# Performance work log

Hardware: AMD Instinct MI355X
Metric: run time of the kernel (lower is better)

Reference implementation:

```python
import jax, jax.numpy as jnp
import numpy as np
from jax import lax

B, C, D, NH, H, W = 32, 768, 512, 4, 24, 24
HD = C // NH          # 192
FHW = H * W           # 576 (must equal 24*24 per o_proj_img2)


def _p(key, shape, scale=0.02):
    return scale * jax.random.normal(key, shape, dtype=jnp.float32)


def setup_inputs() -> dict:
    ks = jax.random.split(jax.random.key(0), 10)
    return dict(
        img_feats=jax.random.normal(ks[0], (B, C, H, W), jnp.float32),
        txt_feats=jax.random.normal(ks[1], (B, D), jnp.float32),
        fn_w=jnp.ones((C,), jnp.float32), fn_b=jnp.zeros((C,), jnp.float32),
        gn_w=jnp.ones((D,), jnp.float32), gn_b=jnp.zeros((D,), jnp.float32),
        qkv_img_w=_p(ks[2], (3 * C, C)),
        qkv_txt_w=_p(ks[3], (3 * C, D)),
        o_img_w=_p(ks[4], (C, C)), o_img_b=jnp.zeros((C,), jnp.float32),
        o_img2_w=_p(ks[5], (FHW, HD)), o_img2_b=jnp.zeros((FHW,), jnp.float32),
        ffn_norm_w=jnp.ones((C,), jnp.float32), ffn_norm_b=jnp.zeros((C,), jnp.float32),
        fc1_w=_p(ks[6], (C, C)),
        dw_w=_p(ks[7], (C, 1, 3, 3)),
        fc2_w=_p(ks[8], (C, C)),
    )


def layernorm2d(x, w, b, eps=1e-6):
    # normalize over channel dim (dim 1) of NCHW
    u = x.mean(1, keepdims=True)
    s = ((x - u) ** 2).mean(1, keepdims=True)
    x = (x - u) * lax.rsqrt(s + eps)
    return w[:, None, None] * x + b[:, None, None]


def l2norm_last(x, eps=1e-12):
    # F.normalize(x, dim=-1): divide by L2 norm clamped at eps
    n = jnp.sqrt(jnp.sum(x * x, axis=-1, keepdims=True))
    return x / jnp.maximum(n, eps)


def _forward(img_feats, txt_feats, fn_w, fn_b, gn_w, gn_b, qkv_img_w, qkv_txt_w,
             o_img_w, o_img_b, o_img2_w, o_img2_b, ffn_norm_w, ffn_norm_b,
             fc1_w, dw_w, fc2_w):
    x = layernorm2d(img_feats, fn_w, fn_b)
    # guide LayerNorm (torch default eps=1e-5, biased var)
    mu = txt_feats.mean(-1, keepdims=True)
    var = jnp.mean((txt_feats - mu) ** 2, axis=-1, keepdims=True)
    t = (txt_feats - mu) * lax.rsqrt(var + 1e-5) * gn_w + gn_b

    # qkv img: 1x1 conv; channel layout (ng nh hd) -> [B,3,NH,HD,F]
    qkv_img = jnp.einsum('bchw,oc->bohw', x, qkv_img_w).reshape(B, 3, NH, HD, FHW)
    q_img, k_img, v_img = qkv_img[:, 0], qkv_img[:, 1], qkv_img[:, 2]

    # qkv txt: layout 'b (nh (ng hd))' per the two rearranges -> [B,NH,3,HD]
    qkv_txt = (t @ qkv_txt_w.T).reshape(B, NH, 3, HD)
    q_txt, k_txt = qkv_txt[:, :, 0], qkv_txt[:, :, 1]

    # normalize over size-1 trailing dim == x / max(|x|, eps)  (sign-like)
    nq_txt = q_txt / jnp.maximum(jnp.abs(q_txt), 1e-12)          # [B,NH,HD]
    nk_img = l2norm_last(k_img)                                  # [B,NH,HD,F]
    # einsum('bnhd,bnhf->bnhf') with d of size 1 == broadcast multiply over h
    attn1 = jax.nn.softmax(nq_txt[..., None] * nk_img, axis=-1)  # [B,NH,HD,F]
    txt_on_img = jnp.einsum('bnhf,bngf->bnhg', attn1, v_img)     # [B,NH,HD,HD]

    nk_txt = k_txt / jnp.maximum(jnp.abs(k_txt), 1e-12)
    nq_img = l2norm_last(q_img)
    attn2 = jax.nn.softmax(nk_txt[..., None] * nq_img, axis=-1)
    txt_to_img2 = jnp.einsum('bnhf,bngf->bnhg', attn2, v_img)

    img = (txt_on_img + txt_to_img2).reshape(B, NH * HD, HD)     # [B,768,192]
    y = (img @ o_img2_w.T + o_img2_b).reshape(B, C, H, W)        # [B,768,24,24]
    out = jnp.einsum('bchw,oc->bohw', y, o_img_w) + o_img_b[None, :, None, None] + img_feats

    # ConvMlp FFN (mlp_times=1, bias=False convs, exact GELU)
    z = layernorm2d(out, ffn_norm_w, ffn_norm_b)
    z = jnp.einsum('bchw,oc->bohw', z, fc1_w)
    z = lax.conv_general_dilated(z, dw_w, (1, 1), 'SAME',
                                 feature_group_count=C,
                                 dimension_numbers=('NCHW', 'OIHW', 'NCHW'))
    z = jax.nn.gelu(z, approximate=False)
    z = jnp.einsum('bchw,oc->bohw', z, fc2_w)
    return out + z


def reference(img_feats, txt_feats, fn_w, fn_b, gn_w, gn_b, qkv_img_w, qkv_txt_w,
              o_img_w, o_img_b, o_img2_w, o_img2_b, ffn_norm_w, ffn_norm_b,
              fc1_w, dw_w, fc2_w):
    return _forward(img_feats, txt_feats, fn_w, fn_b, gn_w, gn_b, qkv_img_w,
                    qkv_txt_w, o_img_w, o_img_b, o_img2_w, o_img2_b,
                    ffn_norm_w, ffn_norm_b, fc1_w, dw_w, fc2_w)
```

## Files before the change

### kernel.cpp

```cpp
#include <hip/hip_runtime.h>

typedef unsigned short u16;
typedef __attribute__((ext_vector_type(8))) short short8_t;
typedef __attribute__((ext_vector_type(4))) float f32x4;

static constexpr int cB   = 32;
static constexpr int cC   = 768;
static constexpr int cD   = 512;
static constexpr int cNH  = 4;
static constexpr int cHD  = 192;
static constexpr int cFHW = 576;
static constexpr int cC3  = 2304;

__device__ inline float us2f(u16 s) {
    union { unsigned int u; float f; } v; v.u = ((unsigned int)s) << 16; return v.f;
}
__device__ inline u16 f2bf(float f) {
    union { float f; unsigned int u; } v; v.f = f;
    unsigned int r = v.u + 0x7FFFu + ((v.u >> 16) & 1u);
    return (u16)(r >> 16);
}
__device__ inline float ldflex(const void* p, size_t i, int isf32) {
    return isf32 ? ((const float*)p)[i] : us2f(((const u16*)p)[i]);
}

__device__ inline void gload16(const void* g, void* l) {
    __builtin_amdgcn_global_load_lds(
        (const __attribute__((address_space(1))) void*)g,
        (__attribute__((address_space(3))) void*)l, 16, 0, 0);
}

__global__ void detect_kernel(const u16* __restrict__ raw, int* __restrict__ flags) {
    flags[0] = (raw[0] == 0x3F80u) ? 0 : 1;
}

struct FlatDesc { const void* src[12]; float* dst[12]; int off[13]; };
__global__ __launch_bounds__(256) void flatten_kernel(FlatDesc d, const int* __restrict__ flags) {
    const int isf = flags[0];
    const int gid = blockIdx.x * 256 + threadIdx.x;
    if (gid >= d.off[12]) return;
    int s = 0;
    #pragma unroll
    for (int i = 1; i < 12; i++) s += (gid >= d.off[i]) ? 1 : 0;
    const int j = gid - d.off[s];
    d.dst[s][j] = ldflex(d.src[s], j, isf);
}

__global__ __launch_bounds__(256) void cast_bf16_kernel(
    const void* __restrict__ src, u16* __restrict__ dst, int n, const int* __restrict__ flags)
{
    const int isf = flags[0];
    for (int i = blockIdx.x * 256 + threadIdx.x; i < n; i += gridDim.x * 256)
        dst[i] = isf ? f2bf(((const float*)src)[i]) : ((const u16*)src)[i];
}

__global__ __launch_bounds__(256) void transpose_kernel(
    const void* __restrict__ src, float* __restrict__ dst,
    int Mdim, int Kdim, const int* __restrict__ flags)
{
    __shared__ float t[32][33];
    const int isf = flags[0];
    const int k0 = blockIdx.x * 32, m0 = blockIdx.y * 32;
    const int x = threadIdx.x & 31, y = threadIdx.x >> 5;
    #pragma unroll
    for (int i = 0; i < 4; i++) {
        const int m = y + i * 8;
        t[m][x] = ldflex(src, (size_t)(m0 + m) * Kdim + k0 + x, isf);
    }
    __syncthreads();
    #pragma unroll
    for (int i = 0; i < 4; i++) {
        const int r = y + i * 8;
        dst[(size_t)(k0 + r) * Mdim + m0 + x] = t[x][r];
    }
}

__global__ __launch_bounds__(256) void txt_ln_kernel(
    const float* __restrict__ txt, const float* __restrict__ gw, const float* __restrict__ gb,
    float* __restrict__ tln)
{
    __shared__ float red[8];
    const int b = blockIdx.x, tid = threadIdx.x;
    const float v0 = txt[(size_t)b * cD + tid];
    const float v1 = txt[(size_t)b * cD + 256 + tid];
    float s = v0 + v1, ss = v0 * v0 + v1 * v1;
    #pragma unroll
    for (int o = 1; o < 64; o <<= 1) { s += __shfl_xor(s, o, 64); ss += __shfl_xor(ss, o, 64); }
    const int wid = tid >> 6, lane = tid & 63;
    if (lane == 0) { red[wid] = s; red[4 + wid] = ss; }
    __syncthreads();
    s  = red[0] + red[1] + red[2] + red[3];
    ss = red[4] + red[5] + red[6] + red[7];
    const float mean = s * (1.f / cD);
    const float var  = fmaxf(ss * (1.f / cD) - mean * mean, 0.f);
    const float r = rsqrtf(var + 1e-5f);
    tln[(size_t)b * cD + tid]       = (v0 - mean) * r * gw[tid]       + gb[tid];
    tln[(size_t)b * cD + 256 + tid] = (v1 - mean) * r * gw[tid + 256] + gb[tid + 256];
}

__global__ __launch_bounds__(256) void txt_gemm_kernel(
    const float* __restrict__ Wt, const float* __restrict__ tln, float* __restrict__ out)
{
    const int o  = blockIdx.x * 256 + threadIdx.x;
    const int b0 = blockIdx.y * 8;
    __shared__ float t[8][cD];
    for (int i = threadIdx.x; i < 8 * cD; i += 256)
        t[i >> 9][i & (cD - 1)] = tln[(size_t)(b0 + (i >> 9)) * cD + (i & (cD - 1))];
    __syncthreads();
    float acc[8] = {};
    #pragma unroll 2
    for (int k = 0; k < cD; k += 4) {
        const float w0 = Wt[(size_t)(k + 0) * cC3 + o];
        const float w1 = Wt[(size_t)(k + 1) * cC3 + o];
        const float w2 = Wt[(size_t)(k + 2) * cC3 + o];
        const float w3 = Wt[(size_t)(k + 3) * cC3 + o];
        #pragma unroll
        for (int b = 0; b < 8; b++) {
            const float4 tv = *(const float4*)&t[b][k];
            acc[b] += w0 * tv.x + w1 * tv.y + w2 * tv.z + w3 * tv.w;
        }
    }
    #pragma unroll
    for (int b = 0; b < 8; b++) out[(size_t)(b0 + b) * cC3 + o] = acc[b];
}

template <int RAW>
__global__ __launch_bounds__(1024) void ln_stats_kernel(
    const void* __restrict__ x, size_t xoff, float* __restrict__ mr,
    const int* __restrict__ flags)
{
    const int isf = RAW ? flags[0] : 1;
    const int b = blockIdx.y;
    const int l = threadIdx.x & 63;
    const int f = (blockIdx.x << 6) + l;
    const int cg = threadIdx.x >> 6;
    const size_t base = (size_t)b * cC * cFHW + f;
    const size_t rbase = RAW ? (xoff + base) : base;
    float s = 0.f, ss = 0.f;
    for (int c = cg; c < cC; c += 16) {
        float v = RAW ? ldflex(x, rbase + (size_t)c * cFHW, isf)
                      : ((const float*)x)[base + (size_t)c * cFHW];
        s += v; ss += v * v;
    }
    __shared__ float S[16][64], SS[16][64];
    S[cg][l] = s; SS[cg][l] = ss;
    __syncthreads();
    if (threadIdx.x < 64) {
        float su = 0.f, sq = 0.f;
        #pragma unroll
        for (int i = 0; i < 16; i++) { su += S[i][l]; sq += SS[i][l]; }
        const float mean = su * (1.f / cC);
        const float var  = fmaxf(sq * (1.f / cC) - mean * mean, 0.f);
        float* o = mr + ((size_t)b * cFHW + f) * 2;
        o[0] = mean; o[1] = rsqrtf(var + 1e-6f);
    }
}

template <int XSRC>
__global__ __launch_bounds__(256) void prep_xt_kernel(
    const void* __restrict__ X, size_t xoff, u16* __restrict__ Xt,
    const float* __restrict__ mr, const float* __restrict__ lnw, const float* __restrict__ lnb,
    const int* __restrict__ flags)
{
    __shared__ float t[64][33];
    const int isf = (XSRC == 2) ? flags[0] : 1;
    const int f0 = blockIdx.x * 32, c0 = blockIdx.y * 64, b = blockIdx.z;
    const int tid = threadIdx.x;
    const int fx = tid & 31, cy = tid >> 5;
    const size_t base = (size_t)b * cC * cFHW;
    #pragma unroll
    for (int i = 0; i < 8; i++) {
        const int c = c0 + cy + i * 8;
        const size_t ei = base + (size_t)c * cFHW + f0 + fx;
        t[cy + i * 8][fx] = (XSRC == 2) ? ldflex(X, xoff + ei, isf) : ((const float*)X)[ei];
    }
    __syncthreads();
    const int cx = tid & 31, fy = tid >> 5;
    #pragma unroll
    for (int i = 0; i < 4; i++) {
        const int fl = fy + i * 8;
        const int f = f0 + fl;
        float v0 = t[cx * 2][fl], v1 = t[cx * 2 + 1][fl];
        if (XSRC >= 1) {
            const float* mp = mr + ((size_t)b * cFHW + f) * 2;
            const float mean = mp[0], rst = mp[1];
            v0 = (v0 - mean) * rst * lnw[c0 + cx * 2]     + lnb[c0 + cx * 2];
            v1 = (v1 - mean) * rst * lnw[c0 + cx * 2 + 1] + lnb[c0 + cx * 2 + 1];
        }
        const unsigned int pk = (unsigned int)f2bf(v0) | ((unsigned int)f2bf(v1) << 16);
        *(unsigned int*)(Xt + base + (size_t)f * cC + c0 + cx * 2) = pk;
    }
}

template <int EPI>
__global__ __launch_bounds__(256, 2) void conv_mfma(
    const u16* __restrict__ Wb, const u16* __restrict__ Xt,
    float* __restrict__ outp, const float* __restrict__ bias_m,
    const void* __restrict__ resRaw, size_t resOff, const float* __restrict__ resF,
    u16* __restrict__ vout,
    int M, int K, int Mt, const int* __restrict__ flags)
{
    const int nwg = 9 * Mt;
    int wg = blockIdx.x;
    {
        const int q = nwg >> 3, r = nwg & 7, x = wg & 7, idx = wg >> 3;
        wg = (x < r ? x * (q + 1) : r * (q + 1) + (x - r) * q) + idx;
    }
    const int xt = wg / Mt, yt = wg - xt * Mt;
    const int n0 = xt * 64, m0 = yt * 256, b = blockIdx.z;

    __shared__ __align__(16) u16 A_s[2][256 * 64];
    __shared__ __align__(16) u16 B_s[2][64 * 64];

    const int tid = threadIdx.x;
    const int w = tid >> 6, lane = tid & 63, lq = lane >> 4, lr = lane & 15;
    const int l8 = lane >> 3, c8 = lane & 7;
    const int xch = ((c8 ^ l8) << 4);

    const u16* wbase = Wb + (size_t)m0 * K;
    const u16* xbase = Xt + ((size_t)b * cFHW + n0) * K;

    f32x4 acc[4][4];
    #pragma unroll
    for (int i = 0; i < 4; i++)
        #pragma unroll
        for (int j = 0; j < 4; j++)
            acc[i][j] = (f32x4)0.f;

    const int nt = K >> 6;

    #pragma unroll
    for (int j = 0; j < 8; ++j) {
        const int r = w * 64 + j * 8 + l8;
        gload16((const char*)(wbase + (size_t)r * K) + xch, (char*)&A_s[0][(w * 64 + j * 8) * 64]);
    }
    #pragma unroll
    for (int j = 0; j < 2; ++j) {
        const int r = w * 16 + j * 8 + l8;
        gload16((const char*)(xbase + (size_t)r * K) + xch, (char*)&B_s[0][(w * 16 + j * 8) * 64]);
    }

    int buf = 0;
    #pragma unroll 1
    for (int t = 0; t < nt; ++t) {
        if (t + 1 < nt) {
            const int k0 = (t + 1) << 6;
            #pragma unroll
            for (int j = 0; j < 8; ++j) {
                const int r = w * 64 + j * 8 + l8;
                gload16((const char*)(wbase + (size_t)r * K + k0) + xch,
                        (char*)&A_s[buf ^ 1][(w * 64 + j * 8) * 64]);
            }
            #pragma unroll
            for (int j = 0; j < 2; ++j) {
                const int r = w * 16 + j * 8 + l8;
                gload16((const char*)(xbase + (size_t)r * K + k0) + xch,
                        (char*)&B_s[buf ^ 1][(w * 16 + j * 8) * 64]);
            }
            asm volatile("s_waitcnt vmcnt(10)" ::: "memory");
        } else {
            asm volatile("s_waitcnt vmcnt(0)" ::: "memory");
        }
        __builtin_amdgcn_s_barrier();
        __builtin_amdgcn_sched_barrier(0);
        __builtin_amdgcn_s_setprio(1);
        const u16* As = &A_s[buf][0];
        const u16* Bs = &B_s[buf][0];
        #pragma unroll
        for (int kk = 0; kk < 2; kk++) {
            short8_t af[4], bfr[4];
            #pragma unroll
            for (int fm = 0; fm < 4; fm++) {
                const int ml = w * 64 + fm * 16 + lr;
                af[fm] = *(const short8_t*)((const char*)As + ml * 128 + ((kk * 64 + lq * 16) ^ ((lr & 7) << 4)));
            }
            #pragma unroll
            for (int fn = 0; fn < 4; fn++) {
                const int nl = fn * 16 + lr;
                bfr[fn] = *(const short8_t*)((const char*)Bs + nl * 128 + ((kk * 64 + lq * 16) ^ ((lr & 7) << 4)));
            }
            #pragma unroll
            for (int fm = 0; fm < 4; fm++)
                #pragma unroll
                for (int fn = 0; fn < 4; fn++)
                    acc[fm][fn] = __builtin_amdgcn_mfma_f32_16x16x32_bf16(af[fm], bfr[fn], acc[fm][fn], 0, 0, 0);
        }
        __builtin_amdgcn_s_setprio(0);
        __builtin_amdgcn_s_barrier();
        buf ^= 1;
    }

    const int isf = (EPI == 1) ? flags[0] : 1;
    (void)isf;
    if constexpr (EPI == 3) {
        if (m0 >= 2 * cC) {
            const int mb = m0 - 2 * cC + w * 64;
            #pragma unroll
            for (int fm = 0; fm < 4; fm++)
                #pragma unroll
                for (int fn = 0; fn < 4; fn++)
                    #pragma unroll
                    for (int i = 0; i < 4; i++) {
                        const int mm = mb + fm * 16 + lq * 4 + i;
                        vout[((size_t)b * cC + mm) * cFHW + n0 + fn * 16 + lr] = f2bf(acc[fm][fn][i]);
                    }
        } else {
            #pragma unroll
            for (int fm = 0; fm < 4; fm++)
                #pragma unroll
                for (int fn = 0; fn < 4; fn++)
                    #pragma unroll
                    for (int i = 0; i < 4; i++) {
                        const int mm = m0 + w * 64 + fm * 16 + lq * 4 + i;
                        outp[((size_t)b * 2 * cC + mm) * cFHW + n0 + fn * 16 + lr] = acc[fm][fn][i];
                    }
        }
        return;
    }
    #pragma unroll
    for (int fm = 0; fm < 4; fm++) {
        #pragma unroll
        for (int fn = 0; fn < 4; fn++) {
            #pragma unroll
            for (int i = 0; i < 4; i++) {
                const int mm = m0 + w * 64 + fm * 16 + lq * 4 + i;
                const size_t o = ((size_t)b * M + mm) * cFHW + n0 + fn * 16 + lr;
                float vv = acc[fm][fn][i];
                if constexpr (EPI == 1) {
                    vv += bias_m[mm] + ldflex(resRaw, resOff + o, isf);
                } else if constexpr (EPI == 2) {
                    vv += resF[o];
                }
                outp[o] = vv;
            }
        }
    }
}

__global__ __launch_bounds__(64) void attn_p_kernel(
    const float* __restrict__ qk, const float* __restrict__ tq, u16* __restrict__ Pbf)
{
    const int idx = blockIdx.x;
    const int h = idx % cHD;
    const int bn = idx / cHD;
    const int n = bn & 3, b = bn >> 2;
    const int lane = threadIdx.x;
    const float* qrow = qk + ((size_t)b * 2 * cC + n * cHD + h) * cFHW;
    const float* krow = qk + ((size_t)b * 2 * cC + cC + n * cHD + h) * cFHW;
    float ssk = 0.f, mink = 3.0e38f, maxk = -3.0e38f;
    float ssq = 0.f, minq = 3.0e38f, maxq = -3.0e38f;
    for (int f = lane; f < cFHW; f += 64) {
        const float kv = krow[f]; ssk += kv * kv; maxk = fmaxf(maxk, kv); mink = fminf(mink, kv);
        const float qv = qrow[f]; ssq += qv * qv; maxq = fmaxf(maxq, qv); minq = fminf(minq, qv);
    }
    #pragma unroll
    for (int o = 1; o < 64; o <<= 1) {
        ssk += __shfl_xor(ssk, o, 64); ssq += __shfl_xor(ssq, o, 64);
        maxk = fmaxf(maxk, __shfl_xor(maxk, o, 64)); mink = fminf(mink, __shfl_xor(mink, o, 64));
        maxq = fmaxf(maxq, __shfl_xor(maxq, o, 64)); minq = fminf(minq, __shfl_xor(minq, o, 64));
    }
    const float qt = tq[(size_t)b * cC3 + n * 3 * cHD + h];
    const float kt = tq[(size_t)b * cC3 + n * 3 * cHD + cHD + h];
    const float sign1 = qt / fmaxf(fabsf(qt), 1e-12f);
    const float sign2 = kt / fmaxf(fabsf(kt), 1e-12f);
    const float a1 = sign1 / fmaxf(sqrtf(ssk), 1e-12f);
    const float a2 = sign2 / fmaxf(sqrtf(ssq), 1e-12f);
    const float m1 = fmaxf(a1 * maxk, a1 * mink);
    const float m2 = fmaxf(a2 * maxq, a2 * minq);
    float z1 = 0.f, z2 = 0.f;
    for (int f = lane; f < cFHW; f += 64) {
        z1 += expf(a1 * krow[f] - m1);
        z2 += expf(a2 * qrow[f] - m2);
    }
    #pragma unroll
    for (int o = 1; o < 64; o <<= 1) { z1 += __shfl_xor(z1, o, 64); z2 += __shfl_xor(z2, o, 64); }
    const float iz1 = 1.f / z1, iz2 = 1.f / z2;
    u16* prow = Pbf + ((size_t)b * cC + n * cHD + h) * cFHW;
    for (int f = lane; f < cFHW; f += 64) {
        const float pv = expf(a1 * krow[f] - m1) * iz1 + expf(a2 * qrow[f] - m2) * iz2;
        prow[f] = f2bf(pv);
    }
}

__global__ __launch_bounds__(256, 2) void pv_mfma(
    const u16* __restrict__ P, const u16* __restrict__ V, float* __restrict__ img, int nbn)
{
    const int nwg = 3 * nbn;
    int wg = blockIdx.x;
    {
        const int q = nwg >> 3, r = nwg & 7, x = wg & 7, idx = wg >> 3;
        wg = (x < r ? x * (q + 1) : r * (q + 1) + (x - r) * q) + idx;
    }
    const int bn = wg / 3, gt = wg - bn * 3;
    const int g0 = gt * 64;
    const int b = bn >> 2, n = bn & 3;

    __shared__ __align__(16) u16 A_s[2][192 * 64];
    __shared__ __align__(16) u16 B_s[2][64 * 64];

    const int tid = threadIdx.x;
    const int w = tid >> 6, lane = tid & 63, lq = lane >> 4, lr = lane & 15;
    const int l8 = lane >> 3, c8 = lane & 7;
    const int xch = ((c8 ^ l8) << 4);

    const u16* pbase = P + ((size_t)b * cC + n * cHD) * cFHW;
    const u16* vbase = V + ((size_t)b * cC + n * cHD + g0) * cFHW;

    f32x4 acc[3][4];
    #pragma unroll
    for (int i = 0; i < 3; i++)
        #pragma unroll
        for (int j = 0; j < 4; j++)
            acc[i][j] = (f32x4)0.f;

    const int nt = cFHW / 64;

    #pragma unroll
    for (int j = 0; j < 6; ++j) {
        const int r = w * 48 + j * 8 + l8;
        gload16((const char*)(pbase + (size_t)r * cFHW) + xch, (char*)&A_s[0][(w * 48 + j * 8) * 64]);
    }
    #pragma unroll
    for (int j = 0; j < 2; ++j) {
        const int r = w * 16 + j * 8 + l8;
        gload16((const char*)(vbase + (size_t)r * cFHW) + xch, (char*)&B_s[0][(w * 16 + j * 8) * 64]);
    }

    int buf = 0;
    #pragma unroll 1
    for (int t = 0; t < nt; ++t) {
        if (t + 1 < nt) {
            const int k0 = (t + 1) << 6;
            #pragma unroll
            for (int j = 0; j < 6; ++j) {
                const int r = w * 48 + j * 8 + l8;
                gload16((const char*)(pbase + (size_t)r * cFHW + k0) + xch,
                        (char*)&A_s[buf ^ 1][(w * 48 + j * 8) * 64]);
            }
            #pragma unroll
            for (int j = 0; j < 2; ++j) {
                const int r = w * 16 + j * 8 + l8;
                gload16((const char*)(vbase + (size_t)r * cFHW + k0) + xch,
                        (char*)&B_s[buf ^ 1][(w * 16 + j * 8) * 64]);
            }
            asm volatile("s_waitcnt vmcnt(8)" ::: "memory");
        } else {
            asm volatile("s_waitcnt vmcnt(0)" ::: "memory");
        }
        __builtin_amdgcn_s_barrier();
        __builtin_amdgcn_sched_barrier(0);
        __builtin_amdgcn_s_setprio(1);
        const u16* As = &A_s[buf][0];
        const u16* Bs = &B_s[buf][0];
        #pragma unroll
        for (int kk = 0; kk < 2; kk++) {
            short8_t af[3], bfr[4];
            #pragma unroll
            for (int fm = 0; fm < 3; fm++) {
                const int ml = w * 48 + fm * 16 + lr;
                af[fm] = *(const short8_t*)((const char*)As + ml * 128 + ((kk * 64 + lq * 16) ^ ((lr & 7) << 4)));
            }
            #pragma unroll
            for (int fn = 0; fn < 4; fn++) {
                const int nl = fn * 16 + lr;
                bfr[fn] = *(const short8_t*)((const char*)Bs + nl * 128 + ((kk * 64 + lq * 16) ^ ((lr & 7) << 4)));
            }
            #pragma unroll
            for (int fm = 0; fm < 3; fm++)
                #pragma unroll
                for (int fn = 0; fn < 4; fn++)
                    acc[fm][fn] = __builtin_amdgcn_mfma_f32_16x16x32_bf16(af[fm], bfr[fn], acc[fm][fn], 0, 0, 0);
        }
        __builtin_amdgcn_s_setprio(0);
        __builtin_amdgcn_s_barrier();
        buf ^= 1;
    }

    #pragma unroll
    for (int fm = 0; fm < 3; fm++)
        #pragma unroll
        for (int fn = 0; fn < 4; fn++)
            #pragma unroll
            for (int i = 0; i < 4; i++) {
                const int mm = w * 48 + fm * 16 + lq * 4 + i;
                img[((size_t)b * cC + n * cHD + mm) * cHD + g0 + fn * 16 + lr] = acc[fm][fn][i];
            }
}

__global__ __launch_bounds__(256) void y_gemm_xt_kernel(
    const float* __restrict__ A, const float* __restrict__ Bw,
    const float* __restrict__ bias_n, u16* __restrict__ Xt)
{
    const int n0 = blockIdx.x * 64, m0 = blockIdx.y * 64, b = blockIdx.z;
    __shared__ __align__(16) float At[16][68];
    __shared__ __align__(16) float Bt[16][68];
    __shared__ __align__(16) u16 T[64][72];
    const int tid = threadIdx.x;
    const int ty = tid >> 4, tx = tid & 15;
    float acc[4][4] = {};
    for (int k0 = 0; k0 < cHD; k0 += 16) {
        const int col = tid & 15, row = tid >> 4;
        #pragma unroll
        for (int p = 0; p < 4; p++) {
            const int r = row + p * 16;
            At[col][r] = A[((size_t)b * cC + m0 + r) * cHD + k0 + col];
            Bt[col][r] = Bw[(size_t)(n0 + r) * cHD + k0 + col];
        }
        __syncthreads();
        #pragma unroll
        for (int kk = 0; kk < 16; kk++) {
            const float4 av = *(const float4*)&At[kk][ty * 4];
            const float4 bv = *(const float4*)&Bt[kk][tx * 4];
            acc[0][0] += av.x * bv.x; acc[0][1] += av.x * bv.y; acc[0][2] += av.x * bv.z; acc[0][3] += av.x * bv.w;
            acc[1][0] += av.y * bv.x; acc[1][1] += av.y * bv.y; acc[1][2] += av.y * bv.z; acc[1][3] += av.y * bv.w;
            acc[2][0] += av.z * bv.x; acc[2][1] += av.z * bv.y; acc[2][2] += av.z * bv.z; acc[2][3] += av.z * bv.w;
            acc[3][0] += av.w * bv.x; acc[3][1] += av.w * bv.y; acc[3][2] += av.w * bv.z; acc[3][3] += av.w * bv.w;
        }
        __syncthreads();
    }
    #pragma unroll
    for (int i = 0; i < 4; i++)
        #pragma unroll
        for (int j = 0; j < 4; j++)
            T[tx * 4 + j][ty * 4 + i] = f2bf(acc[i][j] + bias_n[n0 + tx * 4 + j]);
    __syncthreads();
    const int row = tid >> 2, ch = tid & 3;
    u16* dst = Xt + ((size_t)b * cFHW + n0 + row) * cC + m0 + ch * 16;
    *(int4*)dst       = *(const int4*)&T[row][ch * 16];
    *(int4*)(dst + 8) = *(const int4*)&T[row][ch * 16 + 8];
}

__global__ __launch_bounds__(576) void dwconv_gelu_kernel(
    const float* __restrict__ X, const float* __restrict__ w, float* __restrict__ Y)
{
    const int c = blockIdx.x, b = blockIdx.y;
    __shared__ float t[26][28];
    const int tid = threadIdx.x;
    float* tf = &t[0][0];
    for (int i = tid; i < 26 * 28; i += 576) tf[i] = 0.f;
    __syncthreads();
    const size_t base = ((size_t)b * cC + c) * cFHW;
    const int x = tid % 24, y = tid / 24;
    t[y + 1][x + 1] = X[base + tid];
    __syncthreads();
    float w9[9];
    #pragma unroll
    for (int j = 0; j < 9; j++) w9[j] = w[c * 9 + j];
    float s = 0.f;
    #pragma unroll
    for (int dy = 0; dy < 3; dy++)
        #pragma unroll
        for (int dx = 0; dx < 3; dx++)
            s += w9[dy * 3 + dx] * t[y + dy][x + dx];
    const float g = 0.5f * s * (1.f + erff(s * 0.70710678118654752f));
    Y[base + tid] = g;
}

extern "C" void kernel_launch(void* const* d_in, const int* in_sizes, int n_in,
                              void* d_out, int out_size, void* d_ws, size_t ws_size,
                              hipStream_t stream)
{
    char* p = (char*)d_ws;
    auto allocB = [&](size_t bytes) { char* r = p; p += (bytes + 255) & ~(size_t)255; return r; };
    float* c_txt   = (float*)allocB((size_t)cB * cD * 4);
    float* c_fnw   = (float*)allocB(cC * 4);
    float* c_fnb   = (float*)allocB(cC * 4);
    float* c_gnw   = (float*)allocB(cD * 4);
    float* c_gnb   = (float*)allocB(cD * 4);
    float* c_oib   = (float*)allocB(cC * 4);
    float* c_oi2w  = (float*)allocB((size_t)cFHW * cHD * 4);
    float* c_oi2b  = (float*)allocB(cFHW * 4);
    float* c_ffnw  = (float*)allocB(cC * 4);
    float* c_ffnb  = (float*)allocB(cC * 4);
    float* c_dw    = (float*)allocB(cC * 9 * 4);
    u16*   w_qkv_bf = (u16*)allocB((size_t)cC3 * cC * 2);
    u16*   w_oi_bf  = (u16*)allocB((size_t)cC * cC * 2);
    u16*   w_fc1_bf = (u16*)allocB((size_t)cC * cC * 2);
    u16*   w_fc2_bf = (u16*)allocB((size_t)cC * cC * 2);
    float* t_qkvtw = (float*)allocB((size_t)cD * cC3 * 4);
    float* tln     = (float*)allocB((size_t)cB * cD * 4);
    int*   flags   = (int*)allocB(256);
    float* tq      = (float*)allocB((size_t)cB * cC3 * 4);
    float* mr1     = (float*)allocB((size_t)cB * cFHW * 2 * 4);
    float* mr2     = (float*)allocB((size_t)cB * cFHW * 2 * 4);
    const size_t fixedBytes = (size_t)(p - (char*)d_ws);
    auto needBytes = [&](int Q) {
        return fixedBytes
             + (size_t)Q * cC * cFHW * 4ull * 2ull
             + (size_t)Q * cC * cHD * 4ull
             + (size_t)Q * cC * cFHW * 2ull
             + (size_t)Q * cC * cFHW * 4ull
             + 8192;
    };
    int Q = 8;
    if (ws_size >= needBytes(32)) Q = 32;
    else if (ws_size >= needBytes(16)) Q = 16;
    const size_t QCF = (size_t)Q * cC * cFHW;
    float* slotA = (float*)allocB(2 * QCF * 4);
    float* slotC = (float*)allocB((size_t)Q * cC * cHD * 4);
    u16*   XtA   = (u16*)allocB(QCF * 2);
    char*  pvreg = allocB(QCF * 4);
    u16*   Pbf = (u16*)pvreg;
    u16*   Vbf = (u16*)(pvreg + QCF * 2);
    float* A0 = slotA, *A1 = slotA + QCF;
    float* A2 = (float*)pvreg;
    (void)in_sizes; (void)n_in; (void)out_size;

    detect_kernel<<<1, 1, 0, stream>>>((const u16*)d_in[2], flags);

    FlatDesc fd;
    const void* srcs[11] = { d_in[1], d_in[2], d_in[3], d_in[4], d_in[5],
                             d_in[9], d_in[10], d_in[11], d_in[12], d_in[13], d_in[15] };
    float* dsts[11]      = { c_txt, c_fnw, c_fnb, c_gnw, c_gnb,
                             c_oib, c_oi2w, c_oi2b, c_ffnw, c_ffnb, c_dw };
    const int ns[11]     = { cB * cD, cC, cC, cD, cD,
                             cC, cFHW * cHD, cFHW, cC, cC, cC * 9 };
    int tot = 0;
    for (int i = 0; i < 11; i++) { fd.src[i] = srcs[i]; fd.dst[i] = dsts[i]; fd.off[i] = tot; tot += ns[i]; }
    fd.src[11] = srcs[0]; fd.dst[11] = dsts[0];
    fd.off[11] = tot; fd.off[12] = tot;
    flatten_kernel<<<(tot + 255) / 256, 256, 0, stream>>>(fd, flags);

    cast_bf16_kernel<<<512, 256, 0, stream>>>(d_in[6],  w_qkv_bf, cC3 * cC, flags);
    cast_bf16_kernel<<<256, 256, 0, stream>>>(d_in[8],  w_oi_bf,  cC * cC, flags);
    cast_bf16_kernel<<<256, 256, 0, stream>>>(d_in[14], w_fc1_bf, cC * cC, flags);
    cast_bf16_kernel<<<256, 256, 0, stream>>>(d_in[16], w_fc2_bf, cC * cC, flags);

    transpose_kernel<<<dim3(cD / 32, cC3 / 32), 256, 0, stream>>>(d_in[7], t_qkvtw, cC3, cD, flags);

    txt_ln_kernel<<<cB, 256, 0, stream>>>(c_txt, c_gnw, c_gnb, tln);
    txt_gemm_kernel<<<dim3(cC3 / 256, cB / 8), 256, 0, stream>>>(t_qkvtw, tln, tq);

    for (int q0 = 0; q0 < cB; q0 += Q) {
        const size_t off = (size_t)q0 * cC * cFHW;
        ln_stats_kernel<1><<<dim3(9, Q), 1024, 0, stream>>>(d_in[0], off, mr1, flags);
        prep_xt_kernel<2><<<dim3(cFHW / 32, cC / 64, Q), 256, 0, stream>>>(
            d_in[0], off, XtA, mr1, c_fnw, c_fnb, flags);
        conv_mfma<3><<<dim3(9 * (cC3 / 256), 1, Q), 256, 0, stream>>>(
            w_qkv_bf, XtA, slotA, nullptr, nullptr, 0, nullptr, Vbf, cC3, cC, cC3 / 256, flags);
        attn_p_kernel<<<Q * cNH * cHD, 64, 0, stream>>>(slotA, tq + (size_t)q0 * cC3, Pbf);
        pv_mfma<<<3 * Q * cNH, 256, 0, stream>>>(Pbf, Vbf, slotC, Q * cNH);
        y_gemm_xt_kernel<<<dim3(9, 12, Q), 256, 0, stream>>>(slotC, c_oi2w, c_oi2b, XtA);
        conv_mfma<1><<<dim3(9 * (cC / 256), 1, Q), 256, 0, stream>>>(
            w_oi_bf, XtA, A0, c_oib, d_in[0], off, nullptr, nullptr, cC, cC, cC / 256, flags);
        ln_stats_kernel<0><<<dim3(9, Q), 1024, 0, stream>>>(A0, 0, mr2, flags);
        prep_xt_kernel<1><<<dim3(cFHW / 32, cC / 64, Q), 256, 0, stream>>>(
            A0, 0, XtA, mr2, c_ffnw, c_ffnb, flags);
        conv_mfma<0><<<dim3(9 * (cC / 256), 1, Q), 256, 0, stream>>>(
            w_fc1_bf, XtA, A2, nullptr, nullptr, 0, nullptr, nullptr, cC, cC, cC / 256, flags);
        dwconv_gelu_kernel<<<dim3(cC, Q), 576, 0, stream>>>(A2, c_dw, A1);
        prep_xt_kernel<0><<<dim3(cFHW / 32, cC / 64, Q), 256, 0, stream>>>(
            A1, 0, XtA, nullptr, nullptr, nullptr, flags);
        conv_mfma<2><<<dim3(9 * (cC / 256), 1, Q), 256, 0, stream>>>(
            w_fc2_bf, XtA, (float*)d_out + off, nullptr, nullptr, 0, A0, nullptr, cC, cC, cC / 256, flags);
    }
}
```

Before: 777.0 us.

## Replace fp32 y GEMM with bf16 MFMA kernel and cache attn_p rows in registers

The fp32 SIMT GEMM that projects the attention output through o_proj_img2 is replaced by a bf16 MFMA kernel. It uses double-buffered, swizzled LDS tiles and writes the transposed bf16 Xt directly. pv_mfma now stores its output in bf16 to halve that intermediate buffer, and the o_img2 weight is cast to bf16 once up front. attn_p_kernel keeps the 9 values per lane in registers and reuses the exponentials instead of reading the rows from global memory three times and computing exp twice. The cost is extra bf16 rounding of the intermediate and of the weight.

```diff
diff --git a/kernel.cpp b/kernel.cpp
--- a/kernel.cpp
+++ b/kernel.cpp
@@ -3,6 +3,7 @@
 typedef unsigned short u16;
 typedef __attribute__((ext_vector_type(8))) short short8_t;
 typedef __attribute__((ext_vector_type(4))) float f32x4;
+typedef __attribute__((ext_vector_type(4))) unsigned short u16x4;
 
 static constexpr int cB   = 32;
 static constexpr int cC   = 768;
@@ -347,11 +348,18 @@
     const int lane = threadIdx.x;
     const float* qrow = qk + ((size_t)b * 2 * cC + n * cHD + h) * cFHW;
     const float* krow = qk + ((size_t)b * 2 * cC + cC + n * cHD + h) * cFHW;
+    float kvr[9], qvr[9];
+    #pragma unroll
+    for (int j = 0; j < 9; j++) {
+        kvr[j] = krow[lane + j * 64];
+        qvr[j] = qrow[lane + j * 64];
+    }
     float ssk = 0.f, mink = 3.0e38f, maxk = -3.0e38f;
     float ssq = 0.f, minq = 3.0e38f, maxq = -3.0e38f;
-    for (int f = lane; f < cFHW; f += 64) {
-        const float kv = krow[f]; ssk += kv * kv; maxk = fmaxf(maxk, kv); mink = fminf(mink, kv);
-        const float qv = qrow[f]; ssq += qv * qv; maxq = fmaxf(maxq, qv); minq = fminf(minq, qv);
+    #pragma unroll
+    for (int j = 0; j < 9; j++) {
+        const float kv = kvr[j]; ssk += kv * kv; maxk = fmaxf(maxk, kv); mink = fminf(mink, kv);
+        const float qv = qvr[j]; ssq += qv * qv; maxq = fmaxf(maxq, qv); minq = fminf(minq, qv);
     }
     #pragma unroll
     for (int o = 1; o < 64; o <<= 1) {
@@ -367,23 +375,24 @@
     const float a2 = sign2 / fmaxf(sqrtf(ssq), 1e-12f);
     const float m1 = fmaxf(a1 * maxk, a1 * mink);
     const float m2 = fmaxf(a2 * maxq, a2 * minq);
+    float e1[9], e2[9];
     float z1 = 0.f, z2 = 0.f;
-    for (int f = lane; f < cFHW; f += 64) {
-        z1 += expf(a1 * krow[f] - m1);
-        z2 += expf(a2 * qrow[f] - m2);
+    #pragma unroll
+    for (int j = 0; j < 9; j++) {
+        e1[j] = expf(a1 * kvr[j] - m1); z1 += e1[j];
+        e2[j] = expf(a2 * qvr[j] - m2); z2 += e2[j];
     }
     #pragma unroll
     for (int o = 1; o < 64; o <<= 1) { z1 += __shfl_xor(z1, o, 64); z2 += __shfl_xor(z2, o, 64); }
     const float iz1 = 1.f / z1, iz2 = 1.f / z2;
     u16* prow = Pbf + ((size_t)b * cC + n * cHD + h) * cFHW;
-    for (int f = lane; f < cFHW; f += 64) {
-        const float pv = expf(a1 * krow[f] - m1) * iz1 + expf(a2 * qrow[f] - m2) * iz2;
-        prow[f] = f2bf(pv);
-    }
+    #pragma unroll
+    for (int j = 0; j < 9; j++)
+        prow[lane + j * 64] = f2bf(e1[j] * iz1 + e2[j] * iz2);
 }
 
 __global__ __launch_bounds__(256, 2) void pv_mfma(
-    const u16* __restrict__ P, const u16* __restrict__ V, float* __restrict__ img, int nbn)
+    const u16* __restrict__ P, const u16* __restrict__ V, u16* __restrict__ img, int nbn)
 {
     const int nwg = 3 * nbn;
     int wg = blockIdx.x;
@@ -483,51 +492,118 @@
             #pragma unroll
             for (int i = 0; i < 4; i++) {
                 const int mm = w * 48 + fm * 16 + lq * 4 + i;
-                img[((size_t)b * cC + n * cHD + mm) * cHD + g0 + fn * 16 + lr] = acc[fm][fn][i];
-            }
-}
-
-__global__ __launch_bounds__(256) void y_gemm_xt_kernel(
-    const float* __restrict__ A, const float* __restrict__ Bw,
+                img[((size_t)b * cC + n * cHD + mm) * cHD + g0 + fn * 16 + lr] = f2bf(acc[fm][fn][i]);
+            }
+}
+
+__global__ __launch_bounds__(256, 2) void y_mfma(
+    const u16* __restrict__ img, const u16* __restrict__ o2w,
     const float* __restrict__ bias_n, u16* __restrict__ Xt)
 {
-    const int n0 = blockIdx.x * 64, m0 = blockIdx.y * 64, b = blockIdx.z;
-    __shared__ __align__(16) float At[16][68];
-    __shared__ __align__(16) float Bt[16][68];
-    __shared__ __align__(16) u16 T[64][72];
+    const int nwg = 9 * 3;
+    int wg = blockIdx.x;
+    {
+        const int q = nwg >> 3, r = nwg & 7, x = wg & 7, idx = wg >> 3;
+        wg = (x < r ? x * (q + 1) : r * (q + 1) + (x - r) * q) + idx;
+    }
+    const int xt = wg / 3, yt = wg - xt * 3;
+    const int n0 = xt * 64, m0 = yt * 256, b = blockIdx.z;
+    constexpr int K = cHD;
+
+    __shared__ __align__(16) u16 A_s[2][256 * 64];
+    __shared__ __align__(16) u16 B_s[2][64 * 64];
+
     const int tid = threadIdx.x;
-    const int ty = tid >> 4, tx = tid & 15;
-    float acc[4][4] = {};
-    for (int k0 = 0; k0 < cHD; k0 += 16) {
-        const int col = tid & 15, row = tid >> 4;
-        #pragma unroll
-        for (int p = 0; p < 4; p++) {
-            const int r = row + p * 16;
-            At[col][r] = A[((size_t)b * cC + m0 + r) * cHD + k0 + col];
-            Bt[col][r] = Bw[(size_t)(n0 + r) * cHD + k0 + col];
-        }
-        __syncthreads();
-        #pragma unroll
-        for (int kk = 0; kk < 16; kk++) {
-            const float4 av = *(const float4*)&At[kk][ty * 4];
-            const float4 bv = *(const float4*)&Bt[kk][tx * 4];
-            acc[0][0] += av.x * bv.x; acc[0][1] += av.x * bv.y; acc[0][2] += av.x * bv.z; acc[0][3] += av.x * bv.w;
-            acc[1][0] += av.y * bv.x; acc[1][1] += av.y * bv.y; acc[1][2] += av.y * bv.z; acc[1][3] += av.y * bv.w;
-            acc[2][0] += av.z * bv.x; acc[2][1] += av.z * bv.y; acc[2][2] += av.z * bv.z; acc[2][3] += av.z * bv.w;
-            acc[3][0] += av.w * bv.x; acc[3][1] += av.w * bv.y; acc[3][2] += av.w * bv.z; acc[3][3] += av.w * bv.w;
-        }
-        __syncthreads();
-    }
+    const int w = tid >> 6, lane = tid & 63, lq = lane >> 4, lr = lane & 15;
+    const int l8 = lane >> 3, c8 = lane & 7;
+    const int xch = ((c8 ^ l8) << 4);
+
+    const u16* abase = img + ((size_t)b * cC + m0) * K;
+    const u16* bbase = o2w + (size_t)n0 * K;
+
+    f32x4 acc[4][4];
     #pragma unroll
     for (int i = 0; i < 4; i++)
         #pragma unroll
         for (int j = 0; j < 4; j++)
-            T[tx * 4 + j][ty * 4 + i] = f2bf(acc[i][j] + bias_n[n0 + tx * 4 + j]);
-    __syncthreads();
-    const int row = tid >> 2, ch = tid & 3;
-    u16* dst = Xt + ((size_t)b * cFHW + n0 + row) * cC + m0 + ch * 16;
-    *(int4*)dst       = *(const int4*)&T[row][ch * 16];
-    *(int4*)(dst + 8) = *(const int4*)&T[row][ch * 16 + 8];
+            acc[i][j] = (f32x4)0.f;
+
+    const int nt = K >> 6;
+
+    #pragma unroll
+    for (int j = 0; j < 8; ++j) {
+        const int r = w * 64 + j * 8 + l8;
+        gload16((const char*)(abase + (size_t)r * K) + xch, (char*)&A_s[0][(w * 64 + j * 8) * 64]);
+    }
+    #pragma unroll
+    for (int j = 0; j < 2; ++j) {
+        const int r = w * 16 + j * 8 + l8;
+        gload16((const char*)(bbase + (size_t)r * K) + xch, (char*)&B_s[0][(w * 16 + j * 8) * 64]);
+    }
+
+    int buf = 0;
+    #pragma unroll 1
+    for (int t = 0; t < nt; ++t) {
+        if (t + 1 < nt) {
+            const int k0 = (t + 1) << 6;
+            #pragma unroll
+            for (int j = 0; j < 8; ++j) {
+                const int r = w * 64 + j * 8 + l8;
+                gload16((const char*)(abase + (size_t)r * K + k0) + xch,
+                        (char*)&A_s[buf ^ 1][(w * 64 + j * 8) * 64]);
+            }
+            #pragma unroll
+            for (int j = 0; j < 2; ++j) {
+                const int r = w * 16 + j * 8 + l8;
+                gload16((const char*)(bbase + (size_t)r * K + k0) + xch,
+                        (char*)&B_s[buf ^ 1][(w * 16 + j * 8) * 64]);
+            }
+            asm volatile("s_waitcnt vmcnt(10)" ::: "memory");
+        } else {
+            asm volatile("s_waitcnt vmcnt(0)" ::: "memory");
+        }
+        __builtin_amdgcn_s_barrier();
+        __builtin_amdgcn_sched_barrier(0);
+        __builtin_amdgcn_s_setprio(1);
+        const u16* As = &A_s[buf][0];
+        const u16* Bs = &B_s[buf][0];
+        #pragma unroll
+        for (int kk = 0; kk < 2; kk++) {
+            short8_t af[4], bfr[4];
+            #pragma unroll
+            for (int fm = 0; fm < 4; fm++) {
+                const int ml = w * 64 + fm * 16 + lr;
+                af[fm] = *(const short8_t*)((const char*)As + ml * 128 + ((kk * 64 + lq * 16) ^ ((lr & 7) << 4)));
+            }
+            #pragma unroll
+            for (int fn = 0; fn < 4; fn++) {
+                const int nl = fn * 16 + lr;
+                bfr[fn] = *(const short8_t*)((const char*)Bs + nl * 128 + ((kk * 64 + lq * 16) ^ ((lr & 7) << 4)));
+            }
+            #pragma unroll
+            for (int fm = 0; fm < 4; fm++)
+                #pragma unroll
+                for (int fn = 0; fn < 4; fn++)
+                    acc[fm][fn] = __builtin_amdgcn_mfma_f32_16x16x32_bf16(af[fm], bfr[fn], acc[fm][fn], 0, 0, 0);
+        }
+        __builtin_amdgcn_s_setprio(0);
+        __builtin_amdgcn_s_barrier();
+        buf ^= 1;
+    }
+
+    #pragma unroll
+    for (int fm = 0; fm < 4; fm++) {
+        #pragma unroll
+        for (int fn = 0; fn < 4; fn++) {
+            const int nn = n0 + fn * 16 + lr;
+            const float bn_ = bias_n[nn];
+            u16x4 pk;
+            #pragma unroll
+            for (int i = 0; i < 4; i++) pk[i] = f2bf(acc[fm][fn][i] + bn_);
+            const int mm = m0 + w * 64 + fm * 16 + lq * 4;
+            *(u16x4*)(Xt + ((size_t)b * cFHW + nn) * cC + mm) = pk;
+        }
+    }
 }
 
 __global__ __launch_bounds__(576) void dwconv_gelu_kernel(
@@ -577,6 +653,7 @@
     u16*   w_oi_bf  = (u16*)allocB((size_t)cC * cC * 2);
     u16*   w_fc1_bf = (u16*)allocB((size_t)cC * cC * 2);
     u16*   w_fc2_bf = (u16*)allocB((size_t)cC * cC * 2);
+    u16*   w_o2w_bf = (u16*)allocB((size_t)cFHW * cHD * 2);
     float* t_qkvtw = (float*)allocB((size_t)cD * cC3 * 4);
     float* tln     = (float*)allocB((size_t)cB * cD * 4);
     int*   flags   = (int*)allocB(256);
@@ -587,7 +664,7 @@
     auto needBytes = [&](int Q) {
         return fixedBytes
              + (size_t)Q * cC * cFHW * 4ull * 2ull
-             + (size_t)Q * cC * cHD * 4ull
+             + (size_t)Q * cC * cHD * 2ull
              + (size_t)Q * cC * cFHW * 2ull
              + (size_t)Q * cC * cFHW * 4ull
              + 8192;
@@ -597,7 +674,7 @@
     else if (ws_size >= needBytes(16)) Q = 16;
     const size_t QCF = (size_t)Q * cC * cFHW;
     float* slotA = (float*)allocB(2 * QCF * 4);
-    float* slotC = (float*)allocB((size_t)Q * cC * cHD * 4);
+    u16*   imgbf = (u16*)allocB((size_t)Q * cC * cHD * 2);
     u16*   XtA   = (u16*)allocB(QCF * 2);
     char*  pvreg = allocB(QCF * 4);
     u16*   Pbf = (u16*)pvreg;
@@ -625,6 +702,7 @@
     cast_bf16_kernel<<<256, 256, 0, stream>>>(d_in[8],  w_oi_bf,  cC * cC, flags);
     cast_bf16_kernel<<<256, 256, 0, stream>>>(d_in[14], w_fc1_bf, cC * cC, flags);
     cast_bf16_kernel<<<256, 256, 0, stream>>>(d_in[16], w_fc2_bf, cC * cC, flags);
+    cast_bf16_kernel<<<128, 256, 0, stream>>>(d_in[10], w_o2w_bf, cFHW * cHD, flags);
 
     transpose_kernel<<<dim3(cD / 32, cC3 / 32), 256, 0, stream>>>(d_in[7], t_qkvtw, cC3, cD, flags);
 
@@ -639,8 +717,8 @@
         conv_mfma<3><<<dim3(9 * (cC3 / 256), 1, Q), 256, 0, stream>>>(
             w_qkv_bf, XtA, slotA, nullptr, nullptr, 0, nullptr, Vbf, cC3, cC, cC3 / 256, flags);
         attn_p_kernel<<<Q * cNH * cHD, 64, 0, stream>>>(slotA, tq + (size_t)q0 * cC3, Pbf);
-        pv_mfma<<<3 * Q * cNH, 256, 0, stream>>>(Pbf, Vbf, slotC, Q * cNH);
-        y_gemm_xt_kernel<<<dim3(9, 12, Q), 256, 0, stream>>>(slotC, c_oi2w, c_oi2b, XtA);
+        pv_mfma<<<3 * Q * cNH, 256, 0, stream>>>(Pbf, Vbf, imgbf, Q * cNH);
+        y_mfma<<<dim3(27, 1, Q), 256, 0, stream>>>(imgbf, w_o2w_bf, c_oi2b, XtA);
         conv_mfma<1><<<dim3(9 * (cC / 256), 1, Q), 256, 0, stream>>>(
             w_oi_bf, XtA, A0, c_oib, d_in[0], off, nullptr, nullptr, cC, cC, cC / 256, flags);
         ln_stats_kernel<0><<<dim3(9, Q), 1024, 0, stream>>>(A0, 0, mr2, flags);
```

New measurement: 674.8 us. 1.15x faster.
